# Kernel optimization log

Hardware: AMD Instinct MI355X
Metric: run time of the kernel (lower is better)

Reference implementation:

```python
import jax, jax.numpy as jnp
import numpy as np

B, S, D_IN = 2, 2048, 1024
H, DH = 16, 64          # num_heads, hidden_size (per-head dim)
D_MODEL = H * DH        # 1024
D_OUT = DH * 8          # 512


def setup_inputs() -> dict:
    key = jax.random.key(0)
    ks = jax.random.split(key, 9)
    s_in = 1.0 / np.sqrt(D_IN)
    s_md = 1.0 / np.sqrt(D_MODEL)
    return {
        "x": jax.random.normal(ks[0], (B, S, D_IN), dtype=jnp.float32),
        "Wq": jax.random.uniform(ks[1], (D_IN, D_MODEL), jnp.float32, -s_in, s_in),
        "bq": jax.random.uniform(ks[2], (D_MODEL,), jnp.float32, -s_in, s_in),
        "Wk": jax.random.uniform(ks[3], (D_IN, D_MODEL), jnp.float32, -s_in, s_in),
        "bk": jax.random.uniform(ks[4], (D_MODEL,), jnp.float32, -s_in, s_in),
        "Wv": jax.random.uniform(ks[5], (D_IN, D_MODEL), jnp.float32, -s_in, s_in),
        "bv": jax.random.uniform(ks[6], (D_MODEL,), jnp.float32, -s_in, s_in),
        "Wo": jax.random.uniform(ks[7], (D_MODEL, D_OUT), jnp.float32, -s_md, s_md),
        "bo": jax.random.uniform(ks[8], (D_OUT,), jnp.float32, -s_md, s_md),
    }


def reference(x, Wq, bq, Wk, bk, Wv, bv, Wo, bo):
    b, s, _ = x.shape
    # QKV projections -> [B, H, S, DH]
    def proj(W, bias):
        y = jnp.einsum("bsd,de->bse", x, W) + bias
        return y.reshape(b, s, H, DH).transpose(0, 2, 1, 3)
    Q, K, V = proj(Wq, bq), proj(Wk, bk), proj(Wv, bv)
    scores = jnp.einsum("bhqd,bhkd->bhqk", Q, K) / jnp.sqrt(jnp.float32(DH))
    weights = jax.nn.softmax(scores, axis=-1)
    attn = jnp.einsum("bhqk,bhkd->bhqd", weights, V)  # [B, H, S, DH]
    attn = attn.transpose(0, 2, 1, 3).reshape(b, s, H * DH)
    return jnp.einsum("bsd,de->bse", attn, Wo) + bo
```

## Files before the change

### kernel.cpp

```cpp
#include <hip/hip_runtime.h>

typedef __attribute__((ext_vector_type(8))) __bf16 bf16x8;
typedef __attribute__((ext_vector_type(4))) __bf16 bf16x4;
typedef __attribute__((ext_vector_type(4))) float f32x4;

#define MFMA16x16x32(A, B, C) __builtin_amdgcn_mfma_f32_16x16x32_bf16(A, B, C, 0, 0, 0)

__device__ __forceinline__ unsigned short f2bf(float f) {
    unsigned int u = __float_as_uint(f);
    u += 0x7fffu + ((u >> 16) & 1u);
    return (unsigned short)(u >> 16);
}

__device__ __forceinline__ unsigned cvtpk_bf16(float lo, float hi) {
    unsigned r;
    asm("v_cvt_pk_bf16_f32 %0, %1, %2" : "=v"(r) : "v"(lo), "v"(hi));
    return r;
}

__device__ __forceinline__ float exp2_hw(float x) {
    float r;
    asm("v_exp_f32 %0, %1" : "=v"(r) : "v"(x));
    return r;
}

__device__ __forceinline__ void gload16(const void* src, void* lds) {
    __builtin_amdgcn_global_load_lds(
        (const __attribute__((address_space(1))) unsigned int*)src,
        (__attribute__((address_space(3))) unsigned int*)lds,
        16, 0, 0);
}

__global__ __launch_bounds__(256) void cvt_x_kernel(const float* __restrict__ x,
                                                    unsigned short* __restrict__ xb) {
    const int i = (blockIdx.x * 256 + threadIdx.x) * 4;
    const float4 v = *(const float4*)(x + i);
    ushort4 o;
    o.x = f2bf(v.x); o.y = f2bf(v.y); o.z = f2bf(v.z); o.w = f2bf(v.w);
    *(ushort4*)(xb + i) = o;
}

__global__ __launch_bounds__(256) void tr_w_kernel(const float* __restrict__ W,
                                                   unsigned short* __restrict__ Wt, int N) {
    __shared__ float tile[32][33];
    const int k0 = blockIdx.x * 32;
    const int n0 = blockIdx.y * 32;
    const int tx = threadIdx.x, ty = threadIdx.y;
#pragma unroll
    for (int i = 0; i < 4; ++i)
        tile[ty + 8 * i][tx] = W[(size_t)(k0 + ty + 8 * i) * N + n0 + tx];
    __syncthreads();
#pragma unroll
    for (int i = 0; i < 4; ++i)
        Wt[(size_t)(n0 + ty + 8 * i) * 1024 + k0 + tx] = f2bf(tile[tx][ty + 8 * i]);
}

__global__ __launch_bounds__(256, 3) void gemm_qkv_kernel(
    const unsigned short* __restrict__ xb,
    const unsigned short* __restrict__ Wqt,
    const unsigned short* __restrict__ Wkt,
    const unsigned short* __restrict__ Wvt,
    const float* __restrict__ bq, const float* __restrict__ bk, const float* __restrict__ bv,
    unsigned short* __restrict__ Qb, unsigned short* __restrict__ Kb, unsigned short* __restrict__ Vt)
{
    __shared__ unsigned short sA[2][128 * 32];
    __shared__ unsigned short sB[2][128 * 32];

    const int tid  = threadIdx.x;
    const int lane = tid & 63;
    const int w    = tid >> 6;
    const int wm   = w >> 1, wn = w & 1;
    const int li   = lane & 15, gg = lane >> 4;

    const int L  = blockIdx.y * 24 + blockIdx.x;
    const int v  = (L & 7) * 96 + (L >> 3);
    const int vx = v >> 5;
    const int vy = v & 31;
    const int m0    = vy * 128;
    const int which = vx >> 3;
    const int nloc0 = (vx & 7) * 128;

    const unsigned short* Wt = (which == 0) ? Wqt : ((which == 1) ? Wkt : Wvt);
    const float* bias        = (which == 0) ? bq  : ((which == 1) ? bk  : bv);
    const float osc          = (which == 0) ? 0.18033688011112042f : 1.0f;

    const int srow = lane >> 2;
    const int schk = lane & 3;

    f32x4 acc[4][4];
#pragma unroll
    for (int i = 0; i < 4; ++i)
#pragma unroll
        for (int j = 0; j < 4; ++j)
            acc[i][j] = (f32x4){0.f, 0.f, 0.f, 0.f};

    int aoff[4], boff[4];
#pragma unroll
    for (int f = 0; f < 4; ++f) {
        const int ra = wm * 64 + f * 16 + li;
        aoff[f] = ra * 32 + ((gg ^ ((ra >> 1) & 3)) * 8);
        const int rb = wn * 64 + f * 16 + li;
        boff[f] = rb * 32 + ((gg ^ ((rb >> 1) & 3)) * 8);
    }

#pragma unroll
    for (int j = 0; j < 2; ++j) {
        const int rl = (w * 2 + j) * 16 + srow;
        const int c  = schk ^ ((rl >> 1) & 3);
        gload16(xb + (size_t)(m0 + rl) * 1024 + c * 8,   sA[0] + (w * 2 + j) * 512);
        gload16(Wt + (size_t)(nloc0 + rl) * 1024 + c * 8, sB[0] + (w * 2 + j) * 512);
    }
    __syncthreads();

    for (int kt = 0; kt < 32; ++kt) {
        const int cur = kt & 1;
        if (kt < 31) {
            const int k1 = (kt + 1) * 32;
#pragma unroll
            for (int j = 0; j < 2; ++j) {
                const int rl = (w * 2 + j) * 16 + srow;
                const int c  = schk ^ ((rl >> 1) & 3);
                gload16(xb + (size_t)(m0 + rl) * 1024 + k1 + c * 8,   sA[cur ^ 1] + (w * 2 + j) * 512);
                gload16(Wt + (size_t)(nloc0 + rl) * 1024 + k1 + c * 8, sB[cur ^ 1] + (w * 2 + j) * 512);
            }
        }
        bf16x8 av[4], bw[4];
#pragma unroll
        for (int f = 0; f < 4; ++f) av[f] = *(const bf16x8*)(sA[cur] + aoff[f]);
#pragma unroll
        for (int f = 0; f < 4; ++f) bw[f] = *(const bf16x8*)(sB[cur] + boff[f]);
#pragma unroll
        for (int mf = 0; mf < 4; ++mf)
#pragma unroll
            for (int nf = 0; nf < 4; ++nf)
                acc[mf][nf] = MFMA16x16x32(av[mf], bw[nf], acc[mf][nf]);
        __syncthreads();
    }

    if (which == 2) {
#pragma unroll
        for (int nf = 0; nf < 4; ++nf) {
            const int nl = nloc0 + wn * 64 + nf * 16 + li;
            const float bi = bias[nl];
            const int h = nl >> 6, d = nl & 63;
#pragma unroll
            for (int mf = 0; mf < 4; ++mf) {
                const int m = m0 + wm * 64 + mf * 16 + gg * 4;
                const int b = m >> 11, s0 = m & 2047;
                ushort4 o;
                o.x = f2bf(acc[mf][nf][0] + bi);
                o.y = f2bf(acc[mf][nf][1] + bi);
                o.z = f2bf(acc[mf][nf][2] + bi);
                o.w = f2bf(acc[mf][nf][3] + bi);
                *(ushort4*)(Vt + (((size_t)(b * 16 + h)) * 64 + d) * 2048 + s0) = o;
            }
        }
    } else {
        unsigned short* dst = (which == 0) ? Qb : Kb;
#pragma unroll
        for (int nf = 0; nf < 4; ++nf) {
            const int nl = nloc0 + wn * 64 + nf * 16 + li;
            const float bi = bias[nl];
            const int h = nl >> 6, d = nl & 63;
#pragma unroll
            for (int mf = 0; mf < 4; ++mf) {
#pragma unroll
                for (int r = 0; r < 4; ++r) {
                    const int m = m0 + wm * 64 + mf * 16 + gg * 4 + r;
                    const int b = m >> 11, s = m & 2047;
                    dst[(((size_t)(b * 16 + h)) * 2048 + s) * 64 + d] = f2bf((acc[mf][nf][r] + bi) * osc);
                }
            }
        }
    }
}

__global__ __launch_bounds__(512, 4) void attn_kernel(
    const unsigned short* __restrict__ Qb,
    const unsigned short* __restrict__ Kb,
    const unsigned short* __restrict__ Vt,
    unsigned short* __restrict__ Ob)
{
    __shared__ unsigned short sK[2][64 * 64];
    __shared__ unsigned short sV[2][64 * 64];
    __shared__ unsigned short sP[8][16 * 64];

    const int tid  = threadIdx.x;
    const int lane = tid & 63;
    const int w    = tid >> 6;
    const int li   = lane & 15, gg = lane >> 4;

    const int L  = blockIdx.y * 16 + blockIdx.x;
    const int v  = (L & 7) * 64 + (L >> 3);
    const int bh = v >> 4;
    const int q0 = (v & 15) * 128 + w * 16;

    const int slot = w * 64 + lane;
    const int srow = slot >> 3;
    const int schk = (slot & 7) ^ (srow & 7);

    char* const sPw = (char*)sP[w];
    const int swz = (li & 7) << 4;

    bf16x8 qf[2];
#pragma unroll
    for (int kk = 0; kk < 2; ++kk) {
        const int q = q0 + li;
        const int d = kk * 32 + gg * 8;
        qf[kk] = *(const bf16x8*)(Qb + ((size_t)bh * 2048 + q) * 64 + d);
    }

    f32x4 acc[4];
#pragma unroll
    for (int df = 0; df < 4; ++df) acc[df] = (f32x4){0.f, 0.f, 0.f, 0.f};
    float m_s = -1e30f, l_s = 0.f;

    gload16(Kb + ((size_t)bh * 2048 + srow) * 64 + schk * 8, sK[0] + slot * 8);
    gload16(Vt + ((size_t)bh * 64 + srow) * 2048 + schk * 8, sV[0] + slot * 8);
    __syncthreads();

    for (int t = 0; t < 32; ++t) {
        const int cur = t & 1;
        if (t < 31) {
            gload16(Kb + ((size_t)bh * 2048 + (t + 1) * 64 + srow) * 64 + schk * 8,
                    sK[cur ^ 1] + slot * 8);
            gload16(Vt + ((size_t)bh * 64 + srow) * 2048 + (t + 1) * 64 + schk * 8,
                    sV[cur ^ 1] + slot * 8);
        }

        bf16x8 kf[4][2];
#pragma unroll
        for (int nf = 0; nf < 4; ++nf)
#pragma unroll
            for (int kk = 0; kk < 2; ++kk) {
                const int n = nf * 16 + li;
                const int ch = kk * 4 + gg;
                kf[nf][kk] = *(const bf16x8*)(sK[cur] + n * 64 + ((ch ^ (n & 7)) * 8));
            }
        f32x4 st[4];
#pragma unroll
        for (int nf = 0; nf < 4; ++nf) {
            st[nf] = (f32x4){0.f, 0.f, 0.f, 0.f};
            st[nf] = MFMA16x16x32(kf[nf][0], qf[0], st[nf]);
            st[nf] = MFMA16x16x32(kf[nf][1], qf[1], st[nf]);
        }

        float t0 = fmaxf(fmaxf(st[0][0], st[0][1]), fmaxf(st[0][2], st[0][3]));
        float t1 = fmaxf(fmaxf(st[1][0], st[1][1]), fmaxf(st[1][2], st[1][3]));
        float t2 = fmaxf(fmaxf(st[2][0], st[2][1]), fmaxf(st[2][2], st[2][3]));
        float t3 = fmaxf(fmaxf(st[3][0], st[3][1]), fmaxf(st[3][2], st[3][3]));
        float tm = fmaxf(fmaxf(t0, t1), fmaxf(t2, t3));
        tm = fmaxf(tm, __shfl_xor(tm, 16, 64));
        tm = fmaxf(tm, __shfl_xor(tm, 32, 64));

        if (!__all(tm - m_s <= 8.0f)) {
            const float mnew = fmaxf(m_s, tm);
            const float alpha = exp2_hw(m_s - mnew);
            m_s = mnew;
            l_s *= alpha;
            float al[4];
#pragma unroll
            for (int r = 0; r < 4; ++r) al[r] = __shfl(alpha, gg * 4 + r, 64);
#pragma unroll
            for (int df = 0; df < 4; ++df)
#pragma unroll
                for (int r = 0; r < 4; ++r)
                    acc[df][r] *= al[r];
        }

        float rs = 0.f;
#pragma unroll
        for (int nf = 0; nf < 4; ++nf)
#pragma unroll
            for (int r = 0; r < 4; ++r) {
                const float p = exp2_hw(st[nf][r] - m_s);
                st[nf][r] = p;
                rs += p;
            }
        rs += __shfl_xor(rs, 16, 64);
        rs += __shfl_xor(rs, 32, 64);
        l_s += rs;

#pragma unroll
        for (int nf = 0; nf < 4; ++nf) {
            uint2 pv;
            pv.x = cvtpk_bf16(st[nf][0], st[nf][1]);
            pv.y = cvtpk_bf16(st[nf][2], st[nf][3]);
            const int byte = (li * 128 + nf * 32 + gg * 8) ^ swz;
            *(uint2*)(sPw + byte) = pv;
        }

        bf16x8 pf[2];
#pragma unroll
        for (int kk = 0; kk < 2; ++kk) {
            const int byte = (li * 128 + kk * 64 + gg * 16) ^ swz;
            pf[kk] = *(const bf16x8*)(sPw + byte);
        }
        bf16x8 vf[4][2];
#pragma unroll
        for (int df = 0; df < 4; ++df)
#pragma unroll
            for (int kk = 0; kk < 2; ++kk) {
                const int n = df * 16 + li;
                const int ch = kk * 4 + gg;
                vf[df][kk] = *(const bf16x8*)(sV[cur] + n * 64 + ((ch ^ (n & 7)) * 8));
            }
#pragma unroll
        for (int df = 0; df < 4; ++df) {
            acc[df] = MFMA16x16x32(pf[0], vf[df][0], acc[df]);
            acc[df] = MFMA16x16x32(pf[1], vf[df][1], acc[df]);
        }
        __syncthreads();
    }

    const int b = bh >> 4, h = bh & 15;
#pragma unroll
    for (int r = 0; r < 4; ++r) {
        const float lbc = __shfl(l_s, gg * 4 + r, 64);
        const float rl = 1.0f / lbc;
        const int q = q0 + gg * 4 + r;
#pragma unroll
        for (int df = 0; df < 4; ++df) {
            const int d = df * 16 + li;
            Ob[(((size_t)b * 2048 + q) * 16 + h) * 64 + d] = f2bf(acc[df][r] * rl);
        }
    }
}

__global__ __launch_bounds__(256, 2) void gemm_out_kernel(
    const unsigned short* __restrict__ attn,
    const unsigned short* __restrict__ Wot,
    const float* __restrict__ bo,
    float* __restrict__ out)
{
    __shared__ unsigned short sA[2][64 * 32];
    __shared__ unsigned short sB[2][128 * 32];

    const int tid  = threadIdx.x;
    const int lane = tid & 63;
    const int w    = tid >> 6;
    const int wm   = w >> 1, wn = w & 1;
    const int li   = lane & 15, gg = lane >> 4;
    const int m0   = blockIdx.y * 64;
    const int n0   = blockIdx.x * 128;

    const int arow = tid >> 2;
    const int acol = tid & 3;

    f32x4 acc[2][4];
#pragma unroll
    for (int i = 0; i < 2; ++i)
#pragma unroll
        for (int j = 0; j < 4; ++j)
            acc[i][j] = (f32x4){0.f, 0.f, 0.f, 0.f};

    int aoff[2], boff[4];
#pragma unroll
    for (int f = 0; f < 2; ++f) {
        const int ra = wm * 32 + f * 16 + li;
        aoff[f] = ra * 32 + ((gg ^ ((ra >> 1) & 3)) * 8);
    }
#pragma unroll
    for (int f = 0; f < 4; ++f) {
        const int rb = wn * 64 + f * 16 + li;
        boff[f] = rb * 32 + ((gg ^ ((rb >> 1) & 3)) * 8);
    }

    {
        const int ca = acol ^ ((arow >> 1) & 3);
        gload16(attn + (size_t)(m0 + arow) * 1024 + ca * 8, sA[0] + tid * 8);
#pragma unroll
        for (int jj = 0; jj < 2; ++jj) {
            const int rb = jj * 64 + arow;
            const int cb = acol ^ ((rb >> 1) & 3);
            gload16(Wot + (size_t)(n0 + rb) * 1024 + cb * 8, sB[0] + (jj * 256 + tid) * 8);
        }
    }
    __syncthreads();

    for (int kt = 0; kt < 32; ++kt) {
        const int cur = kt & 1;
        if (kt < 31) {
            const int k1 = (kt + 1) * 32;
            const int ca = acol ^ ((arow >> 1) & 3);
            gload16(attn + (size_t)(m0 + arow) * 1024 + k1 + ca * 8, sA[cur ^ 1] + tid * 8);
#pragma unroll
            for (int jj = 0; jj < 2; ++jj) {
                const int rb = jj * 64 + arow;
                const int cb = acol ^ ((rb >> 1) & 3);
                gload16(Wot + (size_t)(n0 + rb) * 1024 + k1 + cb * 8, sB[cur ^ 1] + (jj * 256 + tid) * 8);
            }
        }
        bf16x8 av[2], bw[4];
#pragma unroll
        for (int f = 0; f < 2; ++f) av[f] = *(const bf16x8*)(sA[cur] + aoff[f]);
#pragma unroll
        for (int f = 0; f < 4; ++f) bw[f] = *(const bf16x8*)(sB[cur] + boff[f]);
#pragma unroll
        for (int mf = 0; mf < 2; ++mf)
#pragma unroll
            for (int nf = 0; nf < 4; ++nf)
                acc[mf][nf] = MFMA16x16x32(av[mf], bw[nf], acc[mf][nf]);
        __syncthreads();
    }

#pragma unroll
    for (int nf = 0; nf < 4; ++nf) {
        const int n = n0 + wn * 64 + nf * 16 + li;
        const float bi = bo[n];
#pragma unroll
        for (int mf = 0; mf < 2; ++mf) {
#pragma unroll
            for (int r = 0; r < 4; ++r) {
                const int m = m0 + wm * 32 + mf * 16 + gg * 4 + r;
                out[(size_t)m * 512 + n] = acc[mf][nf][r] + bi;
            }
        }
    }
}

extern "C" void kernel_launch(void* const* d_in, const int* in_sizes, int n_in,
                              void* d_out, int out_size, void* d_ws, size_t ws_size,
                              hipStream_t stream) {
    const float* x  = (const float*)d_in[0];
    const float* Wq = (const float*)d_in[1];
    const float* bq = (const float*)d_in[2];
    const float* Wk = (const float*)d_in[3];
    const float* bk = (const float*)d_in[4];
    const float* Wv = (const float*)d_in[5];
    const float* bv = (const float*)d_in[6];
    const float* Wo = (const float*)d_in[7];
    const float* bo = (const float*)d_in[8];
    float* out = (float*)d_out;

    unsigned short* ws  = (unsigned short*)d_ws;
    unsigned short* xb  = ws;
    unsigned short* Wqt = xb  + 4194304;
    unsigned short* Wkt = Wqt + 1048576;
    unsigned short* Wvt = Wkt + 1048576;
    unsigned short* Wot = Wvt + 1048576;
    unsigned short* Qb  = Wot + 524288;
    unsigned short* Kb  = Qb  + 4194304;
    unsigned short* Vt  = Kb  + 4194304;
    unsigned short* attnb = Vt + 4194304;

    cvt_x_kernel<<<dim3(4096), dim3(256), 0, stream>>>(x, xb);
    tr_w_kernel<<<dim3(32, 32), dim3(32, 8), 0, stream>>>(Wq, Wqt, 1024);
    tr_w_kernel<<<dim3(32, 32), dim3(32, 8), 0, stream>>>(Wk, Wkt, 1024);
    tr_w_kernel<<<dim3(32, 32), dim3(32, 8), 0, stream>>>(Wv, Wvt, 1024);
    tr_w_kernel<<<dim3(32, 16), dim3(32, 8), 0, stream>>>(Wo, Wot, 512);
    gemm_qkv_kernel<<<dim3(24, 32), dim3(256), 0, stream>>>(xb, Wqt, Wkt, Wvt,
                                                            bq, bk, bv, Qb, Kb, Vt);
    attn_kernel<<<dim3(16, 32), dim3(512), 0, stream>>>(Qb, Kb, Vt, attnb);
    gemm_out_kernel<<<dim3(4, 64), dim3(256), 0, stream>>>(attnb, Wot, bo, out);
}
```

Baseline: 124.6 us.

## Triple-buffer attention K/V loads with one barrier, MFMA priority, merged weight transposes

Moves the attention kernel from double- to triple-buffered K/V tiles in LDS. Each iteration now uses a vmcnt wait plus a single barrier, and tiles are prefetched two steps ahead, replacing the trailing __syncthreads. MFMA sections are wrapped in s_setprio to favour matrix issue across waves. The four weight-transpose launches are merged into one kernel to cut launch overhead. The extra LDS buffers may lower occupancy, and the wraparound prefetch issues redundant loads on the final iterations.

```diff
diff --git a/kernel.cpp b/kernel.cpp
--- a/kernel.cpp
+++ b/kernel.cpp
@@ -40,11 +40,21 @@
     *(ushort4*)(xb + i) = o;
 }
 
-__global__ __launch_bounds__(256) void tr_w_kernel(const float* __restrict__ W,
-                                                   unsigned short* __restrict__ Wt, int N) {
+__global__ __launch_bounds__(256) void tr_w_all_kernel(
+    const float* __restrict__ Wq, const float* __restrict__ Wk,
+    const float* __restrict__ Wv, const float* __restrict__ Wo,
+    unsigned short* __restrict__ Wqt, unsigned short* __restrict__ Wkt,
+    unsigned short* __restrict__ Wvt, unsigned short* __restrict__ Wot)
+{
     __shared__ float tile[32][33];
+    int y = blockIdx.y;
+    const float* W; unsigned short* Wt; int N;
+    if (y < 32)      { W = Wq; Wt = Wqt; N = 1024; }
+    else if (y < 64) { W = Wk; Wt = Wkt; N = 1024; y -= 32; }
+    else if (y < 96) { W = Wv; Wt = Wvt; N = 1024; y -= 64; }
+    else             { W = Wo; Wt = Wot; N = 512;  y -= 96; }
     const int k0 = blockIdx.x * 32;
-    const int n0 = blockIdx.y * 32;
+    const int n0 = y * 32;
     const int tx = threadIdx.x, ty = threadIdx.y;
 #pragma unroll
     for (int i = 0; i < 4; ++i)
@@ -181,8 +191,8 @@
     const unsigned short* __restrict__ Vt,
     unsigned short* __restrict__ Ob)
 {
-    __shared__ unsigned short sK[2][64 * 64];
-    __shared__ unsigned short sV[2][64 * 64];
+    __shared__ unsigned short sK[3][64 * 64];
+    __shared__ unsigned short sV[3][64 * 64];
     __shared__ unsigned short sP[8][16 * 64];
 
     const int tid  = threadIdx.x;
@@ -202,6 +212,9 @@
     char* const sPw = (char*)sP[w];
     const int swz = (li & 7) << 4;
 
+    const unsigned short* Kbase = Kb + ((size_t)bh * 2048 + srow) * 64 + schk * 8;
+    const unsigned short* Vbase = Vt + ((size_t)bh * 64 + srow) * 2048 + schk * 8;
+
     bf16x8 qf[2];
 #pragma unroll
     for (int kk = 0; kk < 2; ++kk) {
@@ -215,17 +228,21 @@
     for (int df = 0; df < 4; ++df) acc[df] = (f32x4){0.f, 0.f, 0.f, 0.f};
     float m_s = -1e30f, l_s = 0.f;
 
-    gload16(Kb + ((size_t)bh * 2048 + srow) * 64 + schk * 8, sK[0] + slot * 8);
-    gload16(Vt + ((size_t)bh * 64 + srow) * 2048 + schk * 8, sV[0] + slot * 8);
-    __syncthreads();
-
+    gload16(Kbase,        sK[0] + slot * 8);
+    gload16(Vbase,        sV[0] + slot * 8);
+    gload16(Kbase + 4096, sK[1] + slot * 8);
+    gload16(Vbase + 64,   sV[1] + slot * 8);
+
+    int cur = 0;
     for (int t = 0; t < 32; ++t) {
-        const int cur = t & 1;
-        if (t < 31) {
-            gload16(Kb + ((size_t)bh * 2048 + (t + 1) * 64 + srow) * 64 + schk * 8,
-                    sK[cur ^ 1] + slot * 8);
-            gload16(Vt + ((size_t)bh * 64 + srow) * 2048 + (t + 1) * 64 + schk * 8,
-                    sV[cur ^ 1] + slot * 8);
+        asm volatile("s_waitcnt vmcnt(2)" ::: "memory");
+        __builtin_amdgcn_s_barrier();
+
+        {
+            const int tn = (t + 2) & 31;
+            const int b2 = (cur >= 1) ? cur - 1 : cur + 2;
+            gload16(Kbase + (size_t)tn * 4096, sK[b2] + slot * 8);
+            gload16(Vbase + (size_t)tn * 64,   sV[b2] + slot * 8);
         }
 
         bf16x8 kf[4][2];
@@ -238,12 +255,14 @@
                 kf[nf][kk] = *(const bf16x8*)(sK[cur] + n * 64 + ((ch ^ (n & 7)) * 8));
             }
         f32x4 st[4];
+        __builtin_amdgcn_s_setprio(1);
 #pragma unroll
         for (int nf = 0; nf < 4; ++nf) {
             st[nf] = (f32x4){0.f, 0.f, 0.f, 0.f};
             st[nf] = MFMA16x16x32(kf[nf][0], qf[0], st[nf]);
             st[nf] = MFMA16x16x32(kf[nf][1], qf[1], st[nf]);
         }
+        __builtin_amdgcn_s_setprio(0);
 
         float t0 = fmaxf(fmaxf(st[0][0], st[0][1]), fmaxf(st[0][2], st[0][3]));
         float t1 = fmaxf(fmaxf(st[1][0], st[1][1]), fmaxf(st[1][2], st[1][3]));
@@ -305,12 +324,15 @@
                 const int ch = kk * 4 + gg;
                 vf[df][kk] = *(const bf16x8*)(sV[cur] + n * 64 + ((ch ^ (n & 7)) * 8));
             }
+        __builtin_amdgcn_s_setprio(1);
 #pragma unroll
         for (int df = 0; df < 4; ++df) {
             acc[df] = MFMA16x16x32(pf[0], vf[df][0], acc[df]);
             acc[df] = MFMA16x16x32(pf[1], vf[df][1], acc[df]);
         }
-        __syncthreads();
+        __builtin_amdgcn_s_setprio(0);
+
+        cur = (cur == 2) ? 0 : cur + 1;
     }
 
     const int b = bh >> 4, h = bh & 15;
@@ -445,10 +467,8 @@
     unsigned short* attnb = Vt + 4194304;
 
     cvt_x_kernel<<<dim3(4096), dim3(256), 0, stream>>>(x, xb);
-    tr_w_kernel<<<dim3(32, 32), dim3(32, 8), 0, stream>>>(Wq, Wqt, 1024);
-    tr_w_kernel<<<dim3(32, 32), dim3(32, 8), 0, stream>>>(Wk, Wkt, 1024);
-    tr_w_kernel<<<dim3(32, 32), dim3(32, 8), 0, stream>>>(Wv, Wvt, 1024);
-    tr_w_kernel<<<dim3(32, 16), dim3(32, 8), 0, stream>>>(Wo, Wot, 512);
+    tr_w_all_kernel<<<dim3(32, 112), dim3(32, 8), 0, stream>>>(Wq, Wk, Wv, Wo,
+                                                               Wqt, Wkt, Wvt, Wot);
     gemm_qkv_kernel<<<dim3(24, 32), dim3(256), 0, stream>>>(xb, Wqt, Wkt, Wvt,
                                                             bq, bk, bv, Qb, Kb, Vt);
     attn_kernel<<<dim3(16, 32), dim3(512), 0, stream>>>(Qb, Kb, Vt, attnb);
```

New measurement: 121.4 us. 1.03x faster.
